# Kernel optimization log

Measured on AMD Instinct MI355X. Metric: run time of the kernel, lower is better.

The kernel has to match this reference:

```python
import jax, jax.numpy as jnp
import numpy as np

NUM_CLASSES = 80
MASK_SIZE = 3
ATTRIBS = 5 + NUM_CLASSES
NET_W = 608.0
NET_H = 608.0
# Faithful to the original indexing bug: anchor_w = masked_anchors[a], anchor_h = masked_anchors[a+1]
MASKED_ANCHORS = np.array([10.0, 13.0, 16.0, 30.0, 33.0, 23.0], dtype=np.float32)
ANCHOR_W = jnp.asarray(MASKED_ANCHORS[0:MASK_SIZE])      # [10, 13, 16]
ANCHOR_H = jnp.asarray(MASKED_ANCHORS[1:MASK_SIZE + 1])  # [13, 16, 30]


def setup_inputs() -> dict:
    key = jax.random.key(0)
    x = jax.random.normal(key, (16, MASK_SIZE * ATTRIBS, 76, 76), dtype=jnp.float32)
    return {"x": x}


def reference(x):
    B, C, H, W = x.shape
    # (B, A, attribs, H, W) -> (B, A, H, W, attribs)
    pred = x.reshape(B, MASK_SIZE, ATTRIBS, H, W).transpose(0, 1, 3, 4, 2)
    tx = jax.nn.sigmoid(pred[..., 0])
    ty = jax.nn.sigmoid(pred[..., 1])
    tw = pred[..., 2]
    th = pred[..., 3]
    conf = jax.nn.sigmoid(pred[..., 4])
    pred_cls = jax.nn.sigmoid(pred[..., 5:])

    gi = jnp.arange(W, dtype=x.dtype)[None, None, None, :]  # column index i
    gj = jnp.arange(H, dtype=x.dtype)[None, None, :, None]  # row index j
    bx = (gi + tx) / W
    by = (gj + ty) / H
    bw = jnp.exp(tw) * ANCHOR_W[None, :, None, None] / NET_W
    bh = jnp.exp(th) * ANCHOR_H[None, :, None, None] / NET_H

    boxes = jnp.stack([bx, by, bw, bh], axis=-1)  # (B, A, H, W, 4)
    # (B, A, H, W, 4+1+num_classes)
    return jnp.concatenate([boxes, conf[..., None], pred_cls], axis=-1)
```

## Files before the change

kernel.cpp:

```cpp
#include <hip/hip_runtime.h>
#include <stdint.h>

#define NB       16
#define NA       3
#define HH_      76
#define WW_      76
#define S_TOT    (HH_ * WW_)
#define ATTR     85
#define TILE_S   76
#define TILES    (S_TOT / TILE_S)
#define NTHREADS 512
#define QUADS    22
#define UNITS1   (QUADS * TILE_S)
#define UNITS2   (TILE_S * ATTR / 4)
#define NB1      4
#define NB2      4
#define LOG2E    1.44269504088896340f

typedef __attribute__((ext_vector_type(4))) float float4v;

__device__ __forceinline__ float fast_sigmoid(float x) {
    float e = __builtin_amdgcn_exp2f(x * (-LOG2E));
    return __builtin_amdgcn_rcpf(1.0f + e);
}

__global__ __launch_bounds__(NTHREADS, 8)
void yolo_layer_kernel(const float* __restrict__ in,
                       float* __restrict__ out) {
    __shared__ __attribute__((aligned(16))) float lds[TILE_S * ATTR];

    const int tid  = threadIdx.x;
    const int tile = blockIdx.x;
    const int BA   = blockIdx.y;
    const int a    = BA % NA;
    const int s0   = tile * TILE_S;

    const float aw = (a == 0) ? 10.0f : (a == 1) ? 13.0f : 16.0f;
    const float ah = (a == 0) ? 13.0f : (a == 1) ? 16.0f : 30.0f;
    const float cw = aw * (1.0f / 608.0f);
    const float ch = ah * (1.0f / 608.0f);

    const float* inb = in + (size_t)BA * (ATTR * S_TOT) + s0;

    float v[NB1][4];
    #pragma unroll
    for (int i = 0; i < NB1; ++i) {
        int u  = tid + i * NTHREADS;
        int uc = (u < UNITS1) ? u : 0;
        int g  = uc / TILE_S;
        int s  = uc - g * TILE_S;
        const float* p = inb + s;
        #pragma unroll
        for (int q = 0; q < 4; ++q) {
            int k = 4 * g + q;
            if (k > ATTR - 1) k = ATTR - 1;
            v[i][q] = p[(size_t)k * S_TOT];
        }
    }

    #pragma unroll
    for (int i = 0; i < NB1; ++i) {
        int u = tid + i * NTHREADS;
        if (u >= UNITS1) break;
        int g = u / TILE_S;
        int s = u - g * TILE_S;

        float r[4];
        if (g != 0) {
            #pragma unroll
            for (int q = 0; q < 4; ++q) r[q] = fast_sigmoid(v[i][q]);
        } else {
            int sp = s0 + s;
            int hy = sp / WW_;
            int wx = sp - hy * WW_;
            r[0] = ((float)wx + fast_sigmoid(v[i][0])) * (1.0f / 76.0f);
            r[1] = ((float)hy + fast_sigmoid(v[i][1])) * (1.0f / 76.0f);
            r[2] = __builtin_amdgcn_exp2f(v[i][2] * LOG2E) * cw;
            r[3] = __builtin_amdgcn_exp2f(v[i][3] * LOG2E) * ch;
        }

        float* lp = &lds[s * ATTR + 4 * g];
        #pragma unroll
        for (int q = 0; q < 4; ++q) {
            if (4 * g + q < ATTR) lp[q] = r[q];
        }
    }

    __syncthreads();

    float4v* outv = (float4v*)(out + ((size_t)BA * S_TOT + s0) * ATTR);
    const float4v* ldsv = (const float4v*)lds;

    float4v w[NB2];
    #pragma unroll
    for (int i = 0; i < NB2; ++i) {
        int u  = tid + i * NTHREADS;
        int uc = (u < UNITS2) ? u : 0;
        w[i] = ldsv[uc];
    }
    #pragma unroll
    for (int i = 0; i < NB2; ++i) {
        int u = tid + i * NTHREADS;
        if (u >= UNITS2) break;
        outv[u] = w[i];
    }
}

extern "C" void kernel_launch(void* const* d_in, const int* in_sizes, int n_in,
                              void* d_out, int out_size, void* d_ws, size_t ws_size,
                              hipStream_t stream) {
    const float* in = (const float*)d_in[0];
    float* out = (float*)d_out;

    dim3 grid(TILES, NB * NA);
    dim3 block(NTHREADS);
    yolo_layer_kernel<<<grid, block, 0, stream>>>(in, out);
}
```

Before: 168.7 us.

## Stage input tile into LDS via global_load_lds and compute during output pass

Input tiles now go straight from global memory into LDS using the asynchronous global_load_lds builtin. Each wave loads 64 contiguous dwords, and a rotated-column layout is used to avoid bank conflicts. The sigmoid/exp math moves to the output phase, where each thread reads four transposed LDS elements and writes a float4. This removes the register round trip and the separate compute pass before the barrier, at the cost of per-element integer div/mod and branchy math in the store loop.

Result: no change. 167.0 us (-1.0%).

```diff
diff --git a/kernel.cpp b/kernel.cpp
--- a/kernel.cpp
+++ b/kernel.cpp
@@ -10,10 +10,12 @@
 #define TILE_S   76
 #define TILES    (S_TOT / TILE_S)
 #define NTHREADS 512
-#define QUADS    22
-#define UNITS1   (QUADS * TILE_S)
-#define UNITS2   (TILE_S * ATTR / 4)
-#define NB1      4
+#define NWAVES   (NTHREADS / 64)
+#define TW       (ATTR * TILE_S)
+#define NSTG     ((TW + 63) / 64)
+#define NSTGW    ((NSTG + NWAVES - 1) / NWAVES)
+#define LDSW     (NSTG * 64)
+#define UNITS2   (TW / 4)
 #define NB2      4
 #define LOG2E    1.44269504088896340f
 
@@ -27,9 +29,11 @@
 __global__ __launch_bounds__(NTHREADS, 8)
 void yolo_layer_kernel(const float* __restrict__ in,
                        float* __restrict__ out) {
-    __shared__ __attribute__((aligned(16))) float lds[TILE_S * ATTR];
+    __shared__ __attribute__((aligned(16))) float lds[LDSW];
 
     const int tid  = threadIdx.x;
+    const int lane = tid & 63;
+    const int wv   = tid >> 6;
     const int tile = blockIdx.x;
     const int BA   = blockIdx.y;
     const int a    = BA % NA;
@@ -42,67 +46,56 @@
 
     const float* inb = in + (size_t)BA * (ATTR * S_TOT) + s0;
 
-    float v[NB1][4];
     #pragma unroll
-    for (int i = 0; i < NB1; ++i) {
-        int u  = tid + i * NTHREADS;
-        int uc = (u < UNITS1) ? u : 0;
-        int g  = uc / TILE_S;
-        int s  = uc - g * TILE_S;
-        const float* p = inb + s;
-        #pragma unroll
-        for (int q = 0; q < 4; ++q) {
-            int k = 4 * g + q;
-            if (k > ATTR - 1) k = ATTR - 1;
-            v[i][q] = p[(size_t)k * S_TOT];
+    for (int i = 0; i < NSTGW; ++i) {
+        int j = wv + i * NWAVES;
+        if (j < NSTG) {
+            int p  = j * 64 + lane;
+            int pc = (p < TW) ? p : (TW - 1);
+            int k  = pc / 76;
+            int t  = pc - k * 76;
+            int s  = t - (k >> 2);
+            if (s < 0) s += 76;
+            const float* g = inb + (size_t)k * S_TOT + s;
+            __builtin_amdgcn_global_load_lds(
+                (const __attribute__((address_space(1))) void*)g,
+                (__attribute__((address_space(3))) void*)&lds[j * 64],
+                4, 0, 0);
         }
     }
-
-    #pragma unroll
-    for (int i = 0; i < NB1; ++i) {
-        int u = tid + i * NTHREADS;
-        if (u >= UNITS1) break;
-        int g = u / TILE_S;
-        int s = u - g * TILE_S;
-
-        float r[4];
-        if (g != 0) {
-            #pragma unroll
-            for (int q = 0; q < 4; ++q) r[q] = fast_sigmoid(v[i][q]);
-        } else {
-            int sp = s0 + s;
-            int hy = sp / WW_;
-            int wx = sp - hy * WW_;
-            r[0] = ((float)wx + fast_sigmoid(v[i][0])) * (1.0f / 76.0f);
-            r[1] = ((float)hy + fast_sigmoid(v[i][1])) * (1.0f / 76.0f);
-            r[2] = __builtin_amdgcn_exp2f(v[i][2] * LOG2E) * cw;
-            r[3] = __builtin_amdgcn_exp2f(v[i][3] * LOG2E) * ch;
-        }
-
-        float* lp = &lds[s * ATTR + 4 * g];
-        #pragma unroll
-        for (int q = 0; q < 4; ++q) {
-            if (4 * g + q < ATTR) lp[q] = r[q];
-        }
-    }
-
     __syncthreads();
 
     float4v* outv = (float4v*)(out + ((size_t)BA * S_TOT + s0) * ATTR);
-    const float4v* ldsv = (const float4v*)lds;
 
-    float4v w[NB2];
-    #pragma unroll
-    for (int i = 0; i < NB2; ++i) {
-        int u  = tid + i * NTHREADS;
-        int uc = (u < UNITS2) ? u : 0;
-        w[i] = ldsv[uc];
-    }
     #pragma unroll
     for (int i = 0; i < NB2; ++i) {
         int u = tid + i * NTHREADS;
         if (u >= UNITS2) break;
-        outv[u] = w[i];
+
+        float r[4];
+        #pragma unroll
+        for (int e = 0; e < 4; ++e) {
+            int idx = 4 * u + e;
+            int s   = idx / 85;
+            int k   = idx - s * 85;
+            int t   = s + (k >> 2);
+            if (t >= 76) t -= 76;
+            float x = lds[k * 76 + t];
+
+            if (k >= 4) {
+                r[e] = fast_sigmoid(x);
+            } else if (k == 0) {
+                r[e] = ((float)s + fast_sigmoid(x)) * (1.0f / 76.0f);
+            } else if (k == 1) {
+                r[e] = ((float)tile + fast_sigmoid(x)) * (1.0f / 76.0f);
+            } else {
+                float ex = __builtin_amdgcn_exp2f(x * LOG2E);
+                r[e] = ex * ((k == 2) ? cw : ch);
+            }
+        }
+
+        float4v w = { r[0], r[1], r[2], r[3] };
+        outv[u] = w;
     }
 }
 
```

## Make kernel persistent with double-buffered LDS to overlap tile loads and stores

Applied to the files above, without the earlier changes.

Replaces the one-tile-per-block grid of 3648 blocks with a persistent grid of 768 blocks, each handling 4 or 5 tiles in a loop. The LDS tile is double-buffered so the next tile's global loads and sigmoid/scatter overlap the current tile's LDS read and global store, with manual sched_barriers and a single s_barrier per tile. This removes per-block launch and tail overhead and hides load latency, at the cost of twice the LDS per block and lower occupancy (launch bounds drop from 8 to 6). The uneven tile count per block may leave some imbalance at the end.

Result: no change. 169.8 us (+0.6%).

```diff
diff --git a/kernel.cpp b/kernel.cpp
--- a/kernel.cpp
+++ b/kernel.cpp
@@ -3,18 +3,15 @@
 
 #define NB       16
 #define NA       3
-#define HH_      76
-#define WW_      76
-#define S_TOT    (HH_ * WW_)
+#define S_TOT    5776
 #define ATTR     85
 #define TILE_S   76
-#define TILES    (S_TOT / TILE_S)
+#define NTILES   3648
+#define NBLK     768
 #define NTHREADS 512
-#define QUADS    22
-#define UNITS1   (QUADS * TILE_S)
-#define UNITS2   (TILE_S * ATTR / 4)
-#define NB1      4
-#define NB2      4
+#define TILEW    (TILE_S * ATTR)
+#define UNITS1   (22 * TILE_S)
+#define UNITS2   (TILEW / 4)
 #define LOG2E    1.44269504088896340f
 
 typedef __attribute__((ext_vector_type(4))) float float4v;
@@ -24,85 +21,104 @@
     return __builtin_amdgcn_rcpf(1.0f + e);
 }
 
-__global__ __launch_bounds__(NTHREADS, 8)
+__global__ __launch_bounds__(NTHREADS, 6)
 void yolo_layer_kernel(const float* __restrict__ in,
                        float* __restrict__ out) {
-    __shared__ __attribute__((aligned(16))) float lds[TILE_S * ATTR];
+    __shared__ __attribute__((aligned(16))) float lds[2][TILEW];
 
-    const int tid  = threadIdx.x;
-    const int tile = blockIdx.x;
-    const int BA   = blockIdx.y;
-    const int a    = BA % NA;
-    const int s0   = tile * TILE_S;
+    const int tid = threadIdx.x;
+    const int b   = blockIdx.x;
+    const int n   = (b < NTILES - 4 * NBLK) ? 5 : 4;
 
-    const float aw = (a == 0) ? 10.0f : (a == 1) ? 13.0f : 16.0f;
-    const float ah = (a == 0) ? 13.0f : (a == 1) ? 16.0f : 30.0f;
-    const float cw = aw * (1.0f / 608.0f);
-    const float ch = ah * (1.0f / 608.0f);
+    float v[4][4];
 
-    const float* inb = in + (size_t)BA * (ATTR * S_TOT) + s0;
+    auto LOADR = [&](int lin) {
+        int tBA = lin / TILE_S;
+        int row = lin - tBA * TILE_S;
+        const float* inb = in + (size_t)tBA * (ATTR * S_TOT) + row * TILE_S;
+        #pragma unroll
+        for (int i = 0; i < 4; ++i) {
+            int u  = tid + i * NTHREADS;
+            int uc = (u < UNITS1) ? u : 0;
+            int g  = uc / TILE_S;
+            int s  = uc - g * TILE_S;
+            const float* p = inb + s;
+            #pragma unroll
+            for (int q = 0; q < 4; ++q) {
+                int k = 4 * g + q;
+                if (k > 84) k = 84;
+                v[i][q] = p[(size_t)k * S_TOT];
+            }
+        }
+    };
 
-    float v[NB1][4];
-    #pragma unroll
-    for (int i = 0; i < NB1; ++i) {
-        int u  = tid + i * NTHREADS;
-        int uc = (u < UNITS1) ? u : 0;
-        int g  = uc / TILE_S;
-        int s  = uc - g * TILE_S;
-        const float* p = inb + s;
+    auto MATHSCATTER = [&](int lin, int sel) {
+        int tBA = lin / TILE_S;
+        int row = lin - tBA * TILE_S;
+        int ta  = tBA - 3 * (tBA / 3);
+        float aw = (ta == 0) ? 10.0f : (ta == 1) ? 13.0f : 16.0f;
+        float ah = (ta == 0) ? 13.0f : (ta == 1) ? 16.0f : 30.0f;
+        float cw = aw * (1.0f / 608.0f);
+        float ch = ah * (1.0f / 608.0f);
+        float rowf = (float)row;
         #pragma unroll
-        for (int q = 0; q < 4; ++q) {
-            int k = 4 * g + q;
-            if (k > ATTR - 1) k = ATTR - 1;
-            v[i][q] = p[(size_t)k * S_TOT];
+        for (int i = 0; i < 4; ++i) {
+            int u = tid + i * NTHREADS;
+            if (u >= UNITS1) break;
+            int g = u / TILE_S;
+            int s = u - g * TILE_S;
+            float r[4];
+            if (g != 0) {
+                #pragma unroll
+                for (int q = 0; q < 4; ++q) r[q] = fast_sigmoid(v[i][q]);
+            } else {
+                r[0] = ((float)s + fast_sigmoid(v[i][0])) * (1.0f / 76.0f);
+                r[1] = (rowf + fast_sigmoid(v[i][1])) * (1.0f / 76.0f);
+                r[2] = __builtin_amdgcn_exp2f(v[i][2] * LOG2E) * cw;
+                r[3] = __builtin_amdgcn_exp2f(v[i][3] * LOG2E) * ch;
+            }
+            float* lp = &lds[sel][s * ATTR + 4 * g];
+            #pragma unroll
+            for (int q = 0; q < 4; ++q)
+                if (4 * g + q < ATTR) lp[q] = r[q];
         }
-    }
+    };
 
-    #pragma unroll
-    for (int i = 0; i < NB1; ++i) {
-        int u = tid + i * NTHREADS;
-        if (u >= UNITS1) break;
-        int g = u / TILE_S;
-        int s = u - g * TILE_S;
+    auto COMPUTESTORE = [&](int lin, int sel) {
+        const float4v* ldsv = (const float4v*)&lds[sel][0];
+        float4v* outv = (float4v*)out + (size_t)lin * UNITS2;
+        #pragma unroll
+        for (int i = 0; i < 4; ++i) {
+            int u = tid + i * NTHREADS;
+            if (u >= UNITS2) break;
+            float4v w = ldsv[u];
+            outv[u] = w;
+        }
+    };
 
-        float r[4];
-        if (g != 0) {
-            #pragma unroll
-            for (int q = 0; q < 4; ++q) r[q] = fast_sigmoid(v[i][q]);
-        } else {
-            int sp = s0 + s;
-            int hy = sp / WW_;
-            int wx = sp - hy * WW_;
-            r[0] = ((float)wx + fast_sigmoid(v[i][0])) * (1.0f / 76.0f);
-            r[1] = ((float)hy + fast_sigmoid(v[i][1])) * (1.0f / 76.0f);
-            r[2] = __builtin_amdgcn_exp2f(v[i][2] * LOG2E) * cw;
-            r[3] = __builtin_amdgcn_exp2f(v[i][3] * LOG2E) * ch;
+    LOADR(b);
+    __builtin_amdgcn_sched_barrier(0);
+    MATHSCATTER(b, 0);
+    asm volatile("s_waitcnt lgkmcnt(0)" ::: "memory");
+    __builtin_amdgcn_sched_barrier(0);
+    __builtin_amdgcn_s_barrier();
+    __builtin_amdgcn_sched_barrier(0);
+
+    for (int t = 0; t < n; ++t) {
+        int lin = b + t * NBLK;
+        if (t + 1 < n) {
+            LOADR(lin + NBLK);
+            __builtin_amdgcn_sched_barrier(0);
         }
-
-        float* lp = &lds[s * ATTR + 4 * g];
-        #pragma unroll
-        for (int q = 0; q < 4; ++q) {
-            if (4 * g + q < ATTR) lp[q] = r[q];
+        COMPUTESTORE(lin, t & 1);
+        if (t + 1 < n) {
+            __builtin_amdgcn_sched_barrier(0);
+            MATHSCATTER(lin + NBLK, (t + 1) & 1);
+            asm volatile("s_waitcnt lgkmcnt(0)" ::: "memory");
+            __builtin_amdgcn_sched_barrier(0);
+            __builtin_amdgcn_s_barrier();
+            __builtin_amdgcn_sched_barrier(0);
         }
-    }
-
-    __syncthreads();
-
-    float4v* outv = (float4v*)(out + ((size_t)BA * S_TOT + s0) * ATTR);
-    const float4v* ldsv = (const float4v*)lds;
-
-    float4v w[NB2];
-    #pragma unroll
-    for (int i = 0; i < NB2; ++i) {
-        int u  = tid + i * NTHREADS;
-        int uc = (u < UNITS2) ? u : 0;
-        w[i] = ldsv[uc];
-    }
-    #pragma unroll
-    for (int i = 0; i < NB2; ++i) {
-        int u = tid + i * NTHREADS;
-        if (u >= UNITS2) break;
-        outv[u] = w[i];
     }
 }
 
@@ -112,7 +128,7 @@
     const float* in = (const float*)d_in[0];
     float* out = (float*)d_out;
 
-    dim3 grid(TILES, NB * NA);
+    dim3 grid(NBLK);
     dim3 block(NTHREADS);
     yolo_layer_kernel<<<grid, block, 0, stream>>>(in, out);
 }
```
